# Optimization experiments

Measured on AMD Instinct MI355X. Metric: run time of the kernel, lower is better.

Reference implementation:

```python
import jax, jax.numpy as jnp
import numpy as np

N, C, T, V = 32, 128, 256, 25
K = 5  # temporal kernel size; reflect-pad 2*(K-1)//2 = 4 rows on top
EPS = 1e-5


def _inorm(x):
    # InstanceNorm2d(affine=False): normalize each (n,c) plane over (T,V)
    m = jnp.mean(x, axis=(2, 3), keepdims=True)
    v = jnp.var(x, axis=(2, 3), keepdims=True)
    return (x - m) * jax.lax.rsqrt(v + EPS)


def setup_inputs() -> dict:
    key = jax.random.key(0)
    ks = jax.random.split(key, 5)
    x = jax.random.normal(ks[0], (N, C, T, V), jnp.float32)
    PA = jax.random.normal(ks[1], (V, V), jnp.float32)          # learned adjacency
    Wd = jax.random.normal(ks[2], (C, C), jnp.float32) * 0.05    # 1x1 conv weight (O,I)
    bd = jnp.zeros((C,), jnp.float32)
    Wt = jax.random.normal(ks[3], (C, C, K, 1), jnp.float32) * 0.02  # (O,I,Kt,1)
    bt = jnp.zeros((C,), jnp.float32)
    return {"x": x, "PA": PA, "Wd": Wd, "bd": bd, "Wt": Wt, "bt": bt}


def reference(x, PA, Wd, bd, Wt, bt):
    # GCN unit: x.view(N,C*T,V) @ PA == einsum over last (joint) axis
    g = jnp.einsum('nctv,vw->nctw', x, PA)
    # 1x1 conv (channel GEMM) + bias
    y = jnp.einsum('nctv,oc->notv', g, Wd) + bd[None, :, None, None]
    # instance norm + identity residual (in_c == out_c) + relu
    y = jax.nn.relu(_inorm(y) + x)
    # TCN unit: reflection-pad 4 rows on top of T, conv (5,1) stride 1, instance norm
    yp = jnp.pad(y, ((0, 0), (0, 0), (4, 0), (0, 0)), mode='reflect')
    z = jax.lax.conv_general_dilated(
        yp, Wt, window_strides=(1, 1), padding='VALID',
        dimension_numbers=('NCHW', 'OIHW', 'NCHW')) + bt[None, :, None, None]
    z = _inorm(z)
    # outer residual (identity: in_c == out_c, stride == 1) + relu
    return jax.nn.relu(z + x)
```

## Files before the change

kernel.cpp:

```cpp
#include <hip/hip_runtime.h>


typedef unsigned short u16;
typedef unsigned int   u32;

using short8  = __attribute__((ext_vector_type(8))) short;
using floatx4 = __attribute__((ext_vector_type(4))) float;

#define NBATCH 32
#define CH     128
#define TDIM   256
#define VDIM   25
#define KT     5
#define PLANE  6400
#define EPSF   1e-5f
#define INV_PLANE (1.0f/6400.0f)

__device__ __forceinline__ u16 f2bf(float f) {
    u32 u = __float_as_uint(f);
    return (u16)((u + 0x7fffu + ((u >> 16) & 1u)) >> 16);
}
__device__ __forceinline__ float bf2f(u16 h) {
    return __uint_as_float(((u32)h) << 16);
}
__device__ __forceinline__ void gload_lds16(const void* g, void* l) {
    __builtin_amdgcn_global_load_lds(
        (const __attribute__((address_space(1))) u32*)g,
        (__attribute__((address_space(3))) u32*)l, 16, 0, 0);
}

__global__ __launch_bounds__(256) void k0_init(
    const float* __restrict__ Wd, const float* __restrict__ Wt,
    float* __restrict__ statsY, float* __restrict__ statsZ,
    u16* __restrict__ WdB, u16* __restrict__ Wt_b)
{
    int i = blockIdx.x * 256 + threadIdx.x;
    if (i < 8192) {
        statsY[i] = 0.f;
    } else if (i < 16384) {
        statsZ[i - 8192] = 0.f;
    } else if (i < 32768) {
        int j  = i - 16384;
        int sl = j & 31;
        int o  = (j >> 5) & 127;
        int cc = j >> 12;
        WdB[j] = f2bf(Wd[o * CH + cc * 32 + sl]);
    } else {
        int j  = i - 32768;
        int sl = j & 31;
        int o  = (j >> 5) & 127;
        int r2 = j >> 12;
        int tap = r2 % KT;
        int ic  = r2 / KT;
        int il = (((sl >> 3) ^ (o & 3)) << 3) | (sl & 7);
        Wt_b[j] = f2bf(Wt[(o * CH + ic * 32 + il) * KT + tap]);
    }
}

__global__ __launch_bounds__(256) void k1a_gcn(
    const float* __restrict__ x, const float* __restrict__ PA,
    u16* __restrict__ gT, u16* __restrict__ xb, int useXb)
{
    __shared__ __attribute__((aligned(16))) u32 sG[6800];
    __shared__ float sPA[625];

    const int tid   = threadIdx.x;
    const int nic   = blockIdx.y;
    const int chunk = blockIdx.x;
    const int c0    = chunk * 400;
    const int cl    = tid >> 3;
    const int tl    = tid & 7;

    for (int i = tid; i < 625; i += 256) sPA[i] = PA[i];

    const float* xrow = x + (size_t)(nic * 32 + cl) * PLANE + c0 + tl * 50;
    float xr[50];
#pragma unroll
    for (int w = 0; w < 25; ++w) {
        float2 t2 = *(const float2*)(xrow + 2 * w);
        xr[2 * w]     = t2.x;
        xr[2 * w + 1] = t2.y;
    }
    if (useXb) {
        u32* xbd = (u32*)(xb + (size_t)(nic * 32 + cl) * PLANE + c0 + tl * 50);
#pragma unroll
        for (int w = 0; w < 25; ++w)
            xbd[w] = (u32)f2bf(xr[2 * w]) | ((u32)f2bf(xr[2 * w + 1]) << 16);
    }
    __syncthreads();

    u16* sG16 = (u16*)sG;
#pragma unroll
    for (int v = 0; v < VDIM; ++v) {
        float g0 = 0.f, g1 = 0.f;
#pragma unroll
        for (int w = 0; w < VDIM; ++w) {
            float p = sPA[w * VDIM + v];
            g0 += xr[w] * p;
            g1 += xr[25 + w] * p;
        }
        int r0 = tl * 50 + v;
        sG16[r0 * 34 + cl]        = f2bf(g0);
        sG16[(r0 + 25) * 34 + cl] = f2bf(g1);
    }
    __syncthreads();

    u32* outd = (u32*)gT;
    const size_t ob = ((size_t)nic * PLANE + c0) * 16;
    for (int j = tid; j < 6400; j += 256) {
        int r = j >> 4, dw = j & 15;
        int q = dw >> 2, b = dw & 3;
        outd[ob + r * 16 + (((q ^ (r & 3)) << 2) | b)] = sG[r * 17 + dw];
    }
}

__global__ __launch_bounds__(256) void k1b_mfma(
    const u16* __restrict__ gT, const u16* __restrict__ WdB,
    const float* __restrict__ bd,
    u16* __restrict__ y0b, float* __restrict__ statsY)
{
    __shared__ __attribute__((aligned(16))) char lds[16384];

    const int tid  = threadIdx.x;
    const int wave = tid >> 6;
    const int lane = tid & 63;
    const int l    = lane & 15;
    const int quad = lane >> 4;
    const int n    = blockIdx.y;
    const int c0   = blockIdx.x * 128;
    const int wub  = tid & ~63;

    auto stageB = [&](int cc, char* dst) {
        const char* bsrc = (const char*)gT + ((size_t)(n * 4 + cc) * PLANE + c0) * 64;
#pragma unroll
        for (int it = 0; it < 2; ++it)
            gload_lds16(bsrc + (it * 256 + tid) * 16, dst + (it * 256 + wub) * 16);
    };

    stageB(0, lds);
    __syncthreads();

    floatx4 acc[2][8];
#pragma unroll
    for (int a = 0; a < 2; ++a)
#pragma unroll
        for (int b = 0; b < 8; ++b) acc[a][b] = (floatx4){0.f, 0.f, 0.f, 0.f};

    for (int cc = 0; cc < 4; ++cc) {
        char* const sBc = lds + (cc & 1) * 8192;
        char* const sBn = lds + ((cc + 1) & 1) * 8192;

        const char* abase = (const char*)WdB + cc * 8192 + (wave * 32 + l) * 64 + (quad << 4);
        const short8 a0 = *(const short8*)(abase);
        const short8 a1 = *(const short8*)(abase + 16 * 64);
        __builtin_amdgcn_sched_barrier(0);

        if (cc < 3) stageB(cc + 1, sBn);

#pragma unroll
        for (int ct = 0; ct < 8; ++ct) {
            const int r = ct * 16 + l;
            const short8 b = *(const short8*)(sBc + r * 64 + ((quad ^ (r & 3)) << 4));
            acc[0][ct] = __builtin_amdgcn_mfma_f32_16x16x32_bf16(a0, b, acc[0][ct], 0, 0, 0);
            acc[1][ct] = __builtin_amdgcn_mfma_f32_16x16x32_bf16(a1, b, acc[1][ct], 0, 0, 0);
        }
        __syncthreads();
    }

#pragma unroll
    for (int ot = 0; ot < 2; ++ot) {
#pragma unroll
        for (int reg = 0; reg < 4; ++reg) {
            const int o = wave * 32 + ot * 16 + quad * 4 + reg;
            const float bias = bd[o];
            float s1 = 0.f, s2 = 0.f;
            u16* yp = y0b + (size_t)(n * CH + o) * PLANE + c0 + l;
#pragma unroll
            for (int ct = 0; ct < 8; ++ct) {
                float val = acc[ot][ct][reg] + bias;
                yp[ct * 16] = f2bf(val);
                s1 += val; s2 += val * val;
            }
#pragma unroll
            for (int m = 1; m <= 8; m <<= 1) {
                s1 += __shfl_xor(s1, m, 64);
                s2 += __shfl_xor(s2, m, 64);
            }
            if (l == 0) {
                atomicAdd(&statsY[(n * CH + o) * 2 + 0], s1);
                atomicAdd(&statsY[(n * CH + o) * 2 + 1], s2);
            }
        }
    }
}

__global__ __launch_bounds__(256) void k2_yhat(
    const u16* __restrict__ y0b, const float* __restrict__ x,
    const u16* __restrict__ xb, int useXb,
    const float* __restrict__ statsY, u16* __restrict__ yhatT)
{
    __shared__ u32 sT[256 * 17];
    __shared__ float sM[32], sR[32];

    const int tid = threadIdx.x;
    const int nic = blockIdx.y;
    const int n   = nic >> 2, ic = nic & 3;
    const int c0  = blockIdx.x * 256;

    if (tid < 32) {
        float a = statsY[(n * CH + ic * 32 + tid) * 2 + 0];
        float b = statsY[(n * CH + ic * 32 + tid) * 2 + 1];
        float m = a * INV_PLANE;
        sM[tid] = m;
        sR[tid] = rsqrtf(b * INV_PLANE - m * m + EPSF);
    }
    __syncthreads();

    u16* sT16 = (u16*)sT;
#pragma unroll
    for (int k = 0; k < 4; ++k) {
        int j  = k * 256 + tid;
        int ch = j >> 5;
        int cb = (j & 31) << 3;
        int g  = (n * CH + ic * 32 + ch) * PLANE + c0 + cb;
        short8 yv = *(const short8*)(y0b + g);
        float xf[8];
        if (useXb) {
            short8 xv = *(const short8*)(xb + g);
#pragma unroll
            for (int e = 0; e < 8; ++e) xf[e] = bf2f((u16)xv[e]);
        } else {
            const float4* xp = (const float4*)(x + g);
            float4 x0 = xp[0], x1 = xp[1];
            xf[0] = x0.x; xf[1] = x0.y; xf[2] = x0.z; xf[3] = x0.w;
            xf[4] = x1.x; xf[5] = x1.y; xf[6] = x1.z; xf[7] = x1.w;
        }
        float m = sM[ch], r = sR[ch];
        int wp = ((ch >> 1) ^ ((cb >> 3) & 15));
        u16* dst = sT16 + cb * 34 + wp * 2 + (ch & 1);
#pragma unroll
        for (int e = 0; e < 8; ++e)
            dst[e * 34] = f2bf(fmaxf((bf2f((u16)yv[e]) - m) * r + xf[e], 0.f));
    }
    __syncthreads();

    u32* outd = (u32*)yhatT;
    int obase = (nic * PLANE + c0) * 16;
    for (int idx = tid; idx < 4096; idx += 256) {
        int r = idx >> 4, dw = idx & 15;
        int q = dw >> 2, b = dw & 3;
        u32 val = sT[r * 17 + ((dw ^ (r >> 3)) & 15)];
        outd[obase + r * 16 + (((q ^ (r & 3)) << 2) | b)] = val;
    }
}

__global__ __launch_bounds__(256, 2) void k3_mfma(
    const u16* __restrict__ yhatT, const u16* __restrict__ Wt_b,
    const float* __restrict__ bt,
    u16* __restrict__ zb, float* __restrict__ statsZ)
{
    __shared__ __attribute__((aligned(16))) char lds[65536];
    char* const sB = lds;
    char* const sA = lds + 24576;

    const int tid  = threadIdx.x;
    const int wave = tid >> 6;
    const int wr   = wave >> 1;
    const int wc   = wave & 1;
    const int lane = tid & 63;
    const int l    = lane & 15;
    const int quad = lane >> 4;
    const int id   = blockIdx.x;
    const int xcd  = id & 7;
    const int jj   = id >> 3;
    const int n    = xcd * 4 + jj / 25;
    const int blk  = jj % 25;
    const int c0   = blk * 256;
    const int wub  = tid & ~63;

    floatx4 acc[4][8];
#pragma unroll
    for (int a = 0; a < 4; ++a)
#pragma unroll
        for (int b = 0; b < 8; ++b) acc[a][b] = (floatx4){0.f, 0.f, 0.f, 0.f};

    for (int ic = 0; ic < 4; ++ic) {
        __syncthreads();
        const char* asrc = (const char*)(Wt_b + ic * 20480);
#pragma unroll
        for (int it = 0; it < 10; ++it)
            gload_lds16(asrc + (it * 256 + tid) * 16, sA + (it * 256 + wub) * 16);
        const char* bsrc = (const char*)(yhatT + (size_t)(n * 4 + ic) * (PLANE * 32));
        if (blk == 0) {
#pragma unroll
            for (int it = 0; it < 4; ++it)
                gload_lds16(bsrc + (it * 256 + tid) * 16, sB + 6400 + (it * 256 + wub) * 16);
            const u32* bsrcd = (const u32*)bsrc;
            u32* sBd = (u32*)sB;
            for (int idx = tid; idx < 1600; idx += 256) {
                int r = idx >> 4, dw = idx & 15;
                int q = dw >> 2, b = dw & 3;
                int d = 100 - r;
                int tref = (d + 24) / 25;
                int v = r % 25;
                int sc = tref * 25 + v;
                sBd[r * 16 + (((q ^ (r & 3)) << 2) | b)] =
                    bsrcd[sc * 16 + (((q ^ (sc & 3)) << 2) | b)];
            }
        } else {
            const char* bsrc2 = bsrc + (size_t)(c0 - 100) * 64;
#pragma unroll
            for (int it = 0; it < 6; ++it)
                gload_lds16(bsrc2 + (it * 256 + tid) * 16, sB + (it * 256 + wub) * 16);
        }
        __syncthreads();
#pragma unroll
        for (int tap = 0; tap < KT; ++tap) {
            short8 af[4];
#pragma unroll
            for (int ot = 0; ot < 4; ++ot) {
                int ro = wr * 64 + ot * 16 + l;
                af[ot] = *(const short8*)(sA + tap * 8192 + ro * 64 + ((quad ^ (l & 3)) << 4));
            }
#pragma unroll
            for (int ct = 0; ct < 8; ++ct) {
                int r = wc * 128 + ct * 16 + l + tap * 25;
                const short8 b = *(const short8*)(sB + r * 64 + ((quad ^ (r & 3)) << 4));
#pragma unroll
                for (int ot = 0; ot < 4; ++ot)
                    acc[ot][ct] = __builtin_amdgcn_mfma_f32_16x16x32_bf16(af[ot], b, acc[ot][ct], 0, 0, 0);
            }
        }
    }

#pragma unroll
    for (int ot = 0; ot < 4; ++ot) {
#pragma unroll
        for (int reg = 0; reg < 4; ++reg) {
            const int o = wr * 64 + ot * 16 + quad * 4 + reg;
            const float bias = bt[o];
            float s1 = 0.f, s2 = 0.f;
            u16* zp = zb + (size_t)(n * CH + o) * PLANE + c0 + wc * 128 + l;
#pragma unroll
            for (int ct = 0; ct < 8; ++ct) {
                float val = acc[ot][ct][reg] + bias;
                zp[ct * 16] = f2bf(val);
                s1 += val; s2 += val * val;
            }
#pragma unroll
            for (int m = 1; m <= 8; m <<= 1) {
                s1 += __shfl_xor(s1, m, 64);
                s2 += __shfl_xor(s2, m, 64);
            }
            if (l == 0) {
                atomicAdd(&statsZ[(n * CH + o) * 2 + 0], s1);
                atomicAdd(&statsZ[(n * CH + o) * 2 + 1], s2);
            }
        }
    }
}

__global__ __launch_bounds__(256) void k4_final(
    const u16* __restrict__ zb, const float* __restrict__ x,
    const float* __restrict__ statsZ, float* __restrict__ out)
{
    int g = blockIdx.x * 256 + threadIdx.x;
    int p = g / 800;
    float a = statsZ[p * 2 + 0], b = statsZ[p * 2 + 1];
    float m = a * INV_PLANE;
    float r = rsqrtf(b * INV_PLANE - m * m + EPSF);
    short8 zv = *(const short8*)(zb + (size_t)g * 8);
    const float4* xp = (const float4*)x + (size_t)g * 2;
    float4 x0 = xp[0], x1 = xp[1];
    float4 o0, o1;
    o0.x = fmaxf((bf2f((u16)zv[0]) - m) * r + x0.x, 0.f);
    o0.y = fmaxf((bf2f((u16)zv[1]) - m) * r + x0.y, 0.f);
    o0.z = fmaxf((bf2f((u16)zv[2]) - m) * r + x0.z, 0.f);
    o0.w = fmaxf((bf2f((u16)zv[3]) - m) * r + x0.w, 0.f);
    o1.x = fmaxf((bf2f((u16)zv[4]) - m) * r + x1.x, 0.f);
    o1.y = fmaxf((bf2f((u16)zv[5]) - m) * r + x1.y, 0.f);
    o1.z = fmaxf((bf2f((u16)zv[6]) - m) * r + x1.z, 0.f);
    o1.w = fmaxf((bf2f((u16)zv[7]) - m) * r + x1.w, 0.f);
    float4* op = (float4*)out + (size_t)g * 2;
    op[0] = o0;
    op[1] = o1;
}

extern "C" void kernel_launch(void* const* d_in, const int* in_sizes, int n_in,
                              void* d_out, int out_size, void* d_ws, size_t ws_size,
                              hipStream_t stream) {
    const float* x  = (const float*)d_in[0];
    const float* PA = (const float*)d_in[1];
    const float* Wd = (const float*)d_in[2];
    const float* bd = (const float*)d_in[3];
    const float* Wt = (const float*)d_in[4];
    const float* bt = (const float*)d_in[5];
    float* out = (float*)d_out;

    char* wsb = (char*)d_ws;
    u16*   y0b    = (u16*)(wsb);
    u16*   zb     = y0b;
    u16*   gT     = (u16*)(wsb + 52428800);
    u16*   yhatT  = gT;
    float* statsY = (float*)(wsb + 104857600);
    float* statsZ = (float*)(wsb + 104890368);
    u16*   WdB    = (u16*)(wsb + 104923136);
    u16*   Wt_b   = (u16*)(wsb + 104955904);
    u16*   xb     = (u16*)(wsb + 105119744);
    const int useXb = (ws_size >= (size_t)157548544) ? 1 : 0;

    k0_init<<<dim3(448), dim3(256), 0, stream>>>(Wd, Wt, statsY, statsZ, WdB, Wt_b);
    k1a_gcn<<<dim3(16, 128), dim3(256), 0, stream>>>(x, PA, gT, xb, useXb);
    k1b_mfma<<<dim3(50, 32), dim3(256), 0, stream>>>(gT, WdB, bd, y0b, statsY);
    k2_yhat<<<dim3(25, 128), dim3(256), 0, stream>>>(y0b, x, xb, useXb, statsY, yhatT);
    k3_mfma<<<dim3(800), dim3(256), 0, stream>>>(yhatT, Wt_b, bt, zb, statsZ);
    k4_final<<<dim3(12800), dim3(256), 0, stream>>>(zb, x, statsZ, out);
}
```

Measured before the change: 381.5 us.

## Register-prefetch next yhat tile in TCN GEMM, drop bf16 x copy, transpose PA

In the temporal-conv MFMA kernel, the B tile for the next input-channel chunk is prefetched into registers while the current chunk is stored to LDS, with manual waitcnt and barriers, so global latency overlaps compute. The bias is hoisted into registers. The bf16 copy of x written by the GCN kernel and read by k2 is removed, so k2 reads fp32 x directly: one fewer 26MB write but more read bytes in k2. PA is stored transposed and padded in LDS for contiguous per-column reads. The register prefetch adds VGPR pressure and relies on hand-written waitcnt correctness.

Measured after the change: 364.7 us. 4.4% less time.

```diff
diff --git a/kernel.cpp b/kernel.cpp
--- a/kernel.cpp
+++ b/kernel.cpp
@@ -59,10 +59,10 @@
 
 __global__ __launch_bounds__(256) void k1a_gcn(
     const float* __restrict__ x, const float* __restrict__ PA,
-    u16* __restrict__ gT, u16* __restrict__ xb, int useXb)
+    u16* __restrict__ gT)
 {
     __shared__ __attribute__((aligned(16))) u32 sG[6800];
-    __shared__ float sPA[625];
+    __shared__ __attribute__((aligned(16))) float sPA[700];
 
     const int tid   = threadIdx.x;
     const int nic   = blockIdx.y;
@@ -71,7 +71,10 @@
     const int cl    = tid >> 3;
     const int tl    = tid & 7;
 
-    for (int i = tid; i < 625; i += 256) sPA[i] = PA[i];
+    for (int i = tid; i < 700; i += 256) {
+        int v = i / 28, w = i % 28;
+        sPA[i] = (w < VDIM) ? PA[w * VDIM + v] : 0.f;
+    }
 
     const float* xrow = x + (size_t)(nic * 32 + cl) * PLANE + c0 + tl * 50;
     float xr[50];
@@ -81,21 +84,16 @@
         xr[2 * w]     = t2.x;
         xr[2 * w + 1] = t2.y;
     }
-    if (useXb) {
-        u32* xbd = (u32*)(xb + (size_t)(nic * 32 + cl) * PLANE + c0 + tl * 50);
-#pragma unroll
-        for (int w = 0; w < 25; ++w)
-            xbd[w] = (u32)f2bf(xr[2 * w]) | ((u32)f2bf(xr[2 * w + 1]) << 16);
-    }
     __syncthreads();
 
     u16* sG16 = (u16*)sG;
 #pragma unroll
     for (int v = 0; v < VDIM; ++v) {
         float g0 = 0.f, g1 = 0.f;
+        const float* pav = &sPA[v * 28];
 #pragma unroll
         for (int w = 0; w < VDIM; ++w) {
-            float p = sPA[w * VDIM + v];
+            float p = pav[w];
             g0 += xr[w] * p;
             g1 += xr[25 + w] * p;
         }
@@ -196,7 +194,6 @@
 
 __global__ __launch_bounds__(256) void k2_yhat(
     const u16* __restrict__ y0b, const float* __restrict__ x,
-    const u16* __restrict__ xb, int useXb,
     const float* __restrict__ statsY, u16* __restrict__ yhatT)
 {
     __shared__ u32 sT[256 * 17];
@@ -224,17 +221,11 @@
         int cb = (j & 31) << 3;
         int g  = (n * CH + ic * 32 + ch) * PLANE + c0 + cb;
         short8 yv = *(const short8*)(y0b + g);
+        const float4* xp = (const float4*)(x + g);
+        float4 x0 = xp[0], x1 = xp[1];
         float xf[8];
-        if (useXb) {
-            short8 xv = *(const short8*)(xb + g);
-#pragma unroll
-            for (int e = 0; e < 8; ++e) xf[e] = bf2f((u16)xv[e]);
-        } else {
-            const float4* xp = (const float4*)(x + g);
-            float4 x0 = xp[0], x1 = xp[1];
-            xf[0] = x0.x; xf[1] = x0.y; xf[2] = x0.z; xf[3] = x0.w;
-            xf[4] = x1.x; xf[5] = x1.y; xf[6] = x1.z; xf[7] = x1.w;
-        }
+        xf[0] = x0.x; xf[1] = x0.y; xf[2] = x0.z; xf[3] = x0.w;
+        xf[4] = x1.x; xf[5] = x1.y; xf[6] = x1.z; xf[7] = x1.w;
         float m = sM[ch], r = sR[ch];
         int wp = ((ch >> 1) ^ ((cb >> 3) & 15));
         u16* dst = sT16 + cb * 34 + wp * 2 + (ch & 1);
@@ -277,21 +268,59 @@
     const int blk  = jj % 25;
     const int c0   = blk * 256;
     const int wub  = tid & ~63;
+    const bool mainp = (blk != 0);
+
+    float btv[16];
+#pragma unroll
+    for (int ot = 0; ot < 4; ++ot)
+#pragma unroll
+        for (int reg = 0; reg < 4; ++reg)
+            btv[ot * 4 + reg] = bt[wr * 64 + ot * 16 + quad * 4 + reg];
 
     floatx4 acc[4][8];
 #pragma unroll
     for (int a = 0; a < 4; ++a)
 #pragma unroll
         for (int b = 0; b < 8; ++b) acc[a][b] = (floatx4){0.f, 0.f, 0.f, 0.f};
+
+    auto bsrcIC = [&](int ic) -> const char* {
+        return (const char*)yhatT + ((size_t)(n * 4 + ic) * PLANE) * 64
+             + (size_t)(c0 - 100) * 64;
+    };
+
+    short8 breg[6];
+    if (mainp) {
+#pragma unroll
+        for (int it = 0; it < 6; ++it)
+            breg[it] = *(const short8*)(bsrcIC(0) + (it * 256 + tid) * 16);
+    }
 
     for (int ic = 0; ic < 4; ++ic) {
         __syncthreads();
+
         const char* asrc = (const char*)(Wt_b + ic * 20480);
 #pragma unroll
         for (int it = 0; it < 10; ++it)
             gload_lds16(asrc + (it * 256 + tid) * 16, sA + (it * 256 + wub) * 16);
-        const char* bsrc = (const char*)(yhatT + (size_t)(n * 4 + ic) * (PLANE * 32));
-        if (blk == 0) {
+        __builtin_amdgcn_sched_barrier(0);
+
+        if (mainp) {
+#pragma unroll
+            for (int it = 0; it < 6; ++it)
+                *((short8*)(sB + (it * 256 + tid) * 16)) = breg[it];
+            if (ic < 3) {
+                const char* nb = bsrcIC(ic + 1);
+                __builtin_amdgcn_sched_barrier(0);
+#pragma unroll
+                for (int it = 0; it < 6; ++it)
+                    breg[it] = *(const short8*)(nb + (it * 256 + tid) * 16);
+                __builtin_amdgcn_sched_barrier(0);
+                asm volatile("s_waitcnt vmcnt(6) lgkmcnt(0)" ::: "memory");
+            } else {
+                asm volatile("s_waitcnt vmcnt(0) lgkmcnt(0)" ::: "memory");
+            }
+        } else {
+            const char* bsrc = (const char*)yhatT + ((size_t)(n * 4 + ic) * PLANE) * 64;
 #pragma unroll
             for (int it = 0; it < 4; ++it)
                 gload_lds16(bsrc + (it * 256 + tid) * 16, sB + 6400 + (it * 256 + wub) * 16);
@@ -307,13 +336,11 @@
                 sBd[r * 16 + (((q ^ (r & 3)) << 2) | b)] =
                     bsrcd[sc * 16 + (((q ^ (sc & 3)) << 2) | b)];
             }
-        } else {
-            const char* bsrc2 = bsrc + (size_t)(c0 - 100) * 64;
-#pragma unroll
-            for (int it = 0; it < 6; ++it)
-                gload_lds16(bsrc2 + (it * 256 + tid) * 16, sB + (it * 256 + wub) * 16);
-        }
-        __syncthreads();
+            asm volatile("s_waitcnt vmcnt(0) lgkmcnt(0)" ::: "memory");
+        }
+        __builtin_amdgcn_s_barrier();
+        __builtin_amdgcn_sched_barrier(0);
+
 #pragma unroll
         for (int tap = 0; tap < KT; ++tap) {
             short8 af[4];
@@ -338,7 +365,7 @@
 #pragma unroll
         for (int reg = 0; reg < 4; ++reg) {
             const int o = wr * 64 + ot * 16 + quad * 4 + reg;
-            const float bias = bt[o];
+            const float bias = btv[ot * 4 + reg];
             float s1 = 0.f, s2 = 0.f;
             u16* zp = zb + (size_t)(n * CH + o) * PLANE + c0 + wc * 128 + l;
 #pragma unroll
@@ -406,13 +433,11 @@
     float* statsZ = (float*)(wsb + 104890368);
     u16*   WdB    = (u16*)(wsb + 104923136);
     u16*   Wt_b   = (u16*)(wsb + 104955904);
-    u16*   xb     = (u16*)(wsb + 105119744);
-    const int useXb = (ws_size >= (size_t)157548544) ? 1 : 0;
 
     k0_init<<<dim3(448), dim3(256), 0, stream>>>(Wd, Wt, statsY, statsZ, WdB, Wt_b);
-    k1a_gcn<<<dim3(16, 128), dim3(256), 0, stream>>>(x, PA, gT, xb, useXb);
+    k1a_gcn<<<dim3(16, 128), dim3(256), 0, stream>>>(x, PA, gT);
     k1b_mfma<<<dim3(50, 32), dim3(256), 0, stream>>>(gT, WdB, bd, y0b, statsY);
-    k2_yhat<<<dim3(25, 128), dim3(256), 0, stream>>>(y0b, x, xb, useXb, statsY, yhatT);
+    k2_yhat<<<dim3(25, 128), dim3(256), 0, stream>>>(y0b, x, statsY, yhatT);
     k3_mfma<<<dim3(800), dim3(256), 0, stream>>>(yhatT, Wt_b, bt, zb, statsZ);
     k4_final<<<dim3(12800), dim3(256), 0, stream>>>(zb, x, statsZ, out);
 }
```
